# Optimization experiments

Hardware: AMD Instinct MI355X
Metric: run time of the kernel (lower is better)

Reference implementation:

```python
import jax, jax.numpy as jnp
import numpy as np

N = 100_000      # nodes
E = 1_600_000    # edges (avg degree 16)
IN_DIM = 128
HID = 512
NCLS = 64
BN_EPS = 1e-5


def setup_inputs() -> dict:
    key = jax.random.key(0)
    ks = jax.random.split(key, 16)

    def lin(k, fi, fo):
        kw, kb = jax.random.split(k)
        s = 1.0 / np.sqrt(fi)
        return (jax.random.uniform(kw, (fi, fo), jnp.float32, -s, s),
                jax.random.uniform(kb, (fo,), jnp.float32, -s, s))

    W1a, b1a = lin(ks[2], IN_DIM, HID)
    W1b, b1b = lin(ks[3], HID, HID)
    W2a, b2a = lin(ks[4], HID, HID)
    W2b, b2b = lin(ks[5], HID, NCLS)
    return {
        "x": jax.random.normal(ks[0], (N, IN_DIM), jnp.float32),
        "edge_index": jax.random.randint(ks[1], (2, E), 0, N, jnp.int32),
        "g": jnp.zeros((1,), jnp.int32),
        "A_k": jnp.zeros((1,), jnp.int32),
        "D": jnp.zeros((1,), jnp.int32),
        "Kindices": jnp.zeros((1,), jnp.int32),
        "de": jnp.zeros((1,), jnp.int32),
        "M": jnp.zeros((1,), jnp.int32),
        "I": jnp.zeros((1,), jnp.int32),
        "W1a": W1a, "b1a": b1a, "W1b": W1b, "b1b": b1b,
        "gamma1": jnp.ones((HID,), jnp.float32), "beta1": jnp.zeros((HID,), jnp.float32),
        "W2a": W2a, "b2a": b2a, "W2b": W2b, "b2b": b2b,
        "gamma2": jnp.ones((NCLS,), jnp.float32), "beta2": jnp.zeros((NCLS,), jnp.float32),
    }


def _gin_conv(x, src, dst, Wa, ba, Wb, bb):
    # PyG GINConv (eps=0): nn(x + sum_{j in N(i)} x_j); messages x[src] summed at dst
    agg = jax.ops.segment_sum(x[src], dst, num_segments=N)
    h = x + agg
    h = jax.nn.relu(h @ Wa + ba)
    return h @ Wb + bb


def _batchnorm(x, gamma, beta):
    # training-mode BatchNorm1d: batch stats over node dim, biased variance
    mu = jnp.mean(x, axis=0)
    var = jnp.mean(jnp.square(x - mu), axis=0)
    return gamma * (x - mu) * jax.lax.rsqrt(var + BN_EPS) + beta


def reference(x, edge_index, g, A_k, D, Kindices, de, M, I,
              W1a, b1a, W1b, b1b, gamma1, beta1,
              W2a, b2a, W2b, b2b, gamma2, beta2):
    src, dst = edge_index[0], edge_index[1]
    h = jax.nn.selu(_gin_conv(x, src, dst, W1a, b1a, W1b, b1b))
    h = _batchnorm(h, gamma1, beta1)
    # dropout(p=0.5) omitted (eval-mode / deterministic reference)
    h = jax.nn.selu(_gin_conv(h, src, dst, W2a, b2a, W2b, b2b))
    h = _batchnorm(h, gamma2, beta2)
    return jax.nn.softmax(h, axis=1)
```

## Files before the change

### kernel.cpp

```cpp
#include <hip/hip_runtime.h>
#include <hip/hip_bf16.h>

#define N_NODES 100000
#define N_EDGES 1600000
#define IN_DIM 128
#define HID 512
#define NCLS 64

typedef __attribute__((ext_vector_type(8))) short bf16x8;
typedef __attribute__((ext_vector_type(4))) float f32x4;

__device__ inline float bf2f(unsigned short b) {
    unsigned int u = ((unsigned int)b) << 16;
    return __builtin_bit_cast(float, u);
}
__device__ inline unsigned short f2bf(float f) {
    unsigned int u = __builtin_bit_cast(unsigned int, f);
    unsigned int lsb = (u >> 16) & 1u;
    u += 0x7fffu + lsb;
    return (unsigned short)(u >> 16);
}
__device__ inline float selu_f(float x) {
    const float scale = 1.0507009873554805f;
    const float alpha = 1.6732632423543772f;
    return x > 0.f ? scale * x : scale * alpha * (__expf(x) - 1.f);
}
__device__ inline void stb(float* p, float v) { *p = v; }
__device__ inline void stb(unsigned short* p, float v) { *p = f2bf(v); }

__device__ inline void gl_lds16(const void* g, void* l) {
    __builtin_amdgcn_global_load_lds((const __attribute__((address_space(1))) void*)g,
                                     (__attribute__((address_space(3))) void*)l, 16, 0, 0);
}

__global__ __launch_bounds__(256) void k_cast(const float* __restrict__ x,
                                              unsigned short* __restrict__ xb) {
    size_t g = (size_t)blockIdx.x * 256 + threadIdx.x;
    size_t total = (size_t)N_NODES * IN_DIM / 8;
    if (g >= total) return;
    const float4* p = (const float4*)(x + g * 8);
    float4 v0 = p[0], v1 = p[1];
    uint4 o;
    o.x = (unsigned)f2bf(v0.x) | ((unsigned)f2bf(v0.y) << 16);
    o.y = (unsigned)f2bf(v0.z) | ((unsigned)f2bf(v0.w) << 16);
    o.z = (unsigned)f2bf(v1.x) | ((unsigned)f2bf(v1.y) << 16);
    o.w = (unsigned)f2bf(v1.z) | ((unsigned)f2bf(v1.w) << 16);
    ((uint4*)xb)[g] = o;
}

__global__ __launch_bounds__(256) void k_deg(const int* __restrict__ dst, int* __restrict__ deg) {
    int e = blockIdx.x * 256 + threadIdx.x;
    if (e < N_EDGES) atomicAdd(&deg[dst[e]], 1);
}

#define SCAN_NB 98

__global__ __launch_bounds__(256) void k_scan_part(const int* __restrict__ deg, int* __restrict__ part) {
    __shared__ int sd[256];
    int b = blockIdx.x, t = threadIdx.x;
    int i0 = b * 1024 + t * 4;
    int s = 0;
#pragma unroll
    for (int k = 0; k < 4; ++k) if (i0 + k < N_NODES) s += deg[i0 + k];
    sd[t] = s;
    __syncthreads();
    for (int o = 128; o > 0; o >>= 1) {
        if (t < o) sd[t] += sd[t + o];
        __syncthreads();
    }
    if (t == 0) part[b] = sd[0];
}

__global__ __launch_bounds__(128) void k_scan_mid(const int* __restrict__ part, int* __restrict__ base,
                                                  int* __restrict__ off) {
    __shared__ int sp[128];
    int t = threadIdx.x;
    int v = (t < SCAN_NB) ? part[t] : 0;
    sp[t] = v;
    __syncthreads();
    for (int o = 1; o < 128; o <<= 1) {
        int tv = (t >= o) ? sp[t - o] : 0;
        __syncthreads();
        sp[t] += tv;
        __syncthreads();
    }
    if (t < SCAN_NB) base[t] = sp[t] - v;
    if (t == SCAN_NB - 1) off[N_NODES] = sp[t];
}

__global__ __launch_bounds__(256) void k_scan_fin(const int* __restrict__ deg, const int* __restrict__ base,
                                                  int* __restrict__ off, int* __restrict__ pos) {
    __shared__ int sd[256];
    int b = blockIdx.x, t = threadIdx.x;
    int i0 = b * 1024 + t * 4;
    int v[4]; int s = 0;
#pragma unroll
    for (int k = 0; k < 4; ++k) { v[k] = (i0 + k < N_NODES) ? deg[i0 + k] : 0; s += v[k]; }
    sd[t] = s;
    __syncthreads();
    for (int o = 1; o < 256; o <<= 1) {
        int tv = (t >= o) ? sd[t - o] : 0;
        __syncthreads();
        sd[t] += tv;
        __syncthreads();
    }
    int excl = base[b] + sd[t] - s;
#pragma unroll
    for (int k = 0; k < 4; ++k) {
        if (i0 + k < N_NODES) { off[i0 + k] = excl; pos[i0 + k] = excl; excl += v[k]; }
    }
}

__global__ __launch_bounds__(256) void k_fill(const int* __restrict__ src, const int* __restrict__ dst,
                                              int* __restrict__ pos, int* __restrict__ adj) {
    int e = blockIdx.x * 256 + threadIdx.x;
    if (e < N_EDGES) {
        int p = atomicAdd(&pos[dst[e]], 1);
        adj[p] = src[e];
    }
}

__global__ __launch_bounds__(256) void k_pack(const float* __restrict__ W,
                                              unsigned short* __restrict__ Wp, int K, int NC) {
    int idx = blockIdx.x * 256 + threadIdx.x;
    if (idx >= K * NC) return;
    int j = idx & 7;
    int l = (idx >> 3) & 63;
    int t = idx >> 9;
    int KT = K >> 5;
    int kt = t % KT;
    int nt = t / KT;
    int k = kt * 32 + (l >> 4) * 8 + j;
    int n = nt * 16 + (l & 15);
    Wp[idx] = f2bf(W[(size_t)k * NC + n]);
}

__global__ __launch_bounds__(256) void k_packT(const float* __restrict__ W,
                                               unsigned short* __restrict__ WT, int K, int NC) {
    int idx = blockIdx.x * 256 + threadIdx.x;
    if (idx >= K * NC) return;
    int k = idx & (K - 1);
    int n = idx / K;
    WT[idx] = f2bf(W[(size_t)k * NC + n]);
}

__global__ __launch_bounds__(256) void k_agg1(const unsigned short* __restrict__ xb,
                                              const int* __restrict__ off, const int* __restrict__ adj,
                                              unsigned short* __restrict__ A1) {
    int w = (blockIdx.x * 256 + threadIdx.x) >> 6;
    if (w >= N_NODES) return;
    int lane = threadIdx.x & 63;
    unsigned v = ((const unsigned*)(xb + (size_t)w * IN_DIM))[lane];
    float s0 = bf2f((unsigned short)(v & 0xffff));
    float s1 = bf2f((unsigned short)(v >> 16));
    int e0 = off[w], e1 = off[w + 1];
    int e = e0;
    for (; e + 4 <= e1; e += 4) {
        int j0 = adj[e], j1 = adj[e + 1], j2 = adj[e + 2], j3 = adj[e + 3];
        unsigned u0 = ((const unsigned*)(xb + (size_t)j0 * IN_DIM))[lane];
        unsigned u1 = ((const unsigned*)(xb + (size_t)j1 * IN_DIM))[lane];
        unsigned u2 = ((const unsigned*)(xb + (size_t)j2 * IN_DIM))[lane];
        unsigned u3 = ((const unsigned*)(xb + (size_t)j3 * IN_DIM))[lane];
        s0 += bf2f((unsigned short)(u0 & 0xffff)) + bf2f((unsigned short)(u1 & 0xffff)) +
              bf2f((unsigned short)(u2 & 0xffff)) + bf2f((unsigned short)(u3 & 0xffff));
        s1 += bf2f((unsigned short)(u0 >> 16)) + bf2f((unsigned short)(u1 >> 16)) +
              bf2f((unsigned short)(u2 >> 16)) + bf2f((unsigned short)(u3 >> 16));
    }
    for (; e < e1; ++e) {
        unsigned u = ((const unsigned*)(xb + (size_t)adj[e] * IN_DIM))[lane];
        s0 += bf2f((unsigned short)(u & 0xffff));
        s1 += bf2f((unsigned short)(u >> 16));
    }
    ((unsigned*)(A1 + (size_t)w * IN_DIM))[lane] = (unsigned)f2bf(s0) | ((unsigned)f2bf(s1) << 16);
}

__global__ __launch_bounds__(256) void k_aggbn2(const unsigned short* __restrict__ h,
                                                const int* __restrict__ off, const int* __restrict__ adj,
                                                const float* __restrict__ bn,
                                                unsigned short* __restrict__ outb) {
    int w = (blockIdx.x * 256 + threadIdx.x) >> 6;
    if (w >= N_NODES) return;
    int lane = threadIdx.x & 63;
    int fb = blockIdx.y * 256 + lane * 4;
    const unsigned short* hp = h + fb;
    float scl[4], shf[4];
#pragma unroll
    for (int k = 0; k < 4; ++k) {
        scl[k] = bn[2 * HID + fb + k];
        shf[k] = bn[3 * HID + fb + k];
    }
    uint2 v = *(const uint2*)(hp + (size_t)w * HID);
    float s0 = bf2f((unsigned short)(v.x & 0xffff));
    float s1 = bf2f((unsigned short)(v.x >> 16));
    float s2 = bf2f((unsigned short)(v.y & 0xffff));
    float s3 = bf2f((unsigned short)(v.y >> 16));
    int e0 = off[w], e1 = off[w + 1];
    int e = e0;
    for (; e + 4 <= e1; e += 4) {
        int j0 = adj[e], j1 = adj[e + 1], j2 = adj[e + 2], j3 = adj[e + 3];
        uint2 u0 = *(const uint2*)(hp + (size_t)j0 * HID);
        uint2 u1 = *(const uint2*)(hp + (size_t)j1 * HID);
        uint2 u2 = *(const uint2*)(hp + (size_t)j2 * HID);
        uint2 u3 = *(const uint2*)(hp + (size_t)j3 * HID);
        s0 += bf2f((unsigned short)(u0.x & 0xffff)) + bf2f((unsigned short)(u1.x & 0xffff)) +
              bf2f((unsigned short)(u2.x & 0xffff)) + bf2f((unsigned short)(u3.x & 0xffff));
        s1 += bf2f((unsigned short)(u0.x >> 16)) + bf2f((unsigned short)(u1.x >> 16)) +
              bf2f((unsigned short)(u2.x >> 16)) + bf2f((unsigned short)(u3.x >> 16));
        s2 += bf2f((unsigned short)(u0.y & 0xffff)) + bf2f((unsigned short)(u1.y & 0xffff)) +
              bf2f((unsigned short)(u2.y & 0xffff)) + bf2f((unsigned short)(u3.y & 0xffff));
        s3 += bf2f((unsigned short)(u0.y >> 16)) + bf2f((unsigned short)(u1.y >> 16)) +
              bf2f((unsigned short)(u2.y >> 16)) + bf2f((unsigned short)(u3.y >> 16));
    }
    for (; e < e1; ++e) {
        uint2 u = *(const uint2*)(hp + (size_t)adj[e] * HID);
        s0 += bf2f((unsigned short)(u.x & 0xffff));
        s1 += bf2f((unsigned short)(u.x >> 16));
        s2 += bf2f((unsigned short)(u.y & 0xffff));
        s3 += bf2f((unsigned short)(u.y >> 16));
    }
    float dp1 = (float)(e1 - e0 + 1);
    float r0 = s0 * scl[0] + dp1 * shf[0];
    float r1 = s1 * scl[1] + dp1 * shf[1];
    float r2 = s2 * scl[2] + dp1 * shf[2];
    float r3 = s3 * scl[3] + dp1 * shf[3];
    unsigned long long o =
        (unsigned long long)((unsigned)f2bf(r0) | ((unsigned)f2bf(r1) << 16)) |
        ((unsigned long long)((unsigned)f2bf(r2) | ((unsigned)f2bf(r3) << 16)) << 32);
    __builtin_nontemporal_store(o, (unsigned long long*)(outb + (size_t)w * HID + fb));
}

template <int K, int ACT>
__global__ __launch_bounds__(256) void k_tgemm(const unsigned short* __restrict__ A,
                                               const unsigned short* __restrict__ WT,
                                               const float* __restrict__ bias,
                                               unsigned short* __restrict__ Out, int M) {
    constexpr int NC = 512;
    __shared__ __align__(16) char smem[32768];
    const int tid = threadIdx.x;
    const int lane = tid & 63;
    const int w = tid >> 6;
    const int wm = w >> 1, wn = w & 1;
    const int l15 = lane & 15, lg = lane >> 4;
    const int rowbase = blockIdx.y * 128;
    const int colbase = blockIdx.x * 128;

    f32x4 acc[4][4];
#pragma unroll
    for (int i = 0; i < 4; ++i)
#pragma unroll
        for (int j = 0; j < 4; ++j) acc[i][j] = (f32x4)0.f;

    for (int k0 = 0; k0 < K; k0 += 64) {
#pragma unroll
        for (int i = 0; i < 4; ++i) {
            int slot = i * 256 + tid;
            int r = slot >> 3;
            int u = (slot & 7) ^ (r & 7);
            int gr = rowbase + r; if (gr >= M) gr = M - 1;
            gl_lds16(A + (size_t)gr * K + k0 + u * 8, smem + (i * 256 + w * 64) * 16);
        }
#pragma unroll
        for (int i = 0; i < 4; ++i) {
            int slot = i * 256 + tid;
            int c = slot >> 3;
            int u = (slot & 7) ^ (c & 7);
            gl_lds16(WT + (size_t)(colbase + c) * K + k0 + u * 8,
                     smem + 16384 + (i * 256 + w * 64) * 16);
        }
        __syncthreads();
#pragma unroll
        for (int kin = 0; kin < 2; ++kin) {
            bf16x8 af[4], bfr[4];
#pragma unroll
            for (int mi = 0; mi < 4; ++mi) {
                int r = wm * 64 + mi * 16 + l15;
                int u = (kin * 4 + lg) ^ (r & 7);
                af[mi] = *(const bf16x8*)(smem + r * 128 + u * 16);
            }
#pragma unroll
            for (int ni = 0; ni < 4; ++ni) {
                int c = wn * 64 + ni * 16 + l15;
                int u = (kin * 4 + lg) ^ (c & 7);
                bfr[ni] = *(const bf16x8*)(smem + 16384 + c * 128 + u * 16);
            }
#pragma unroll
            for (int mi = 0; mi < 4; ++mi)
#pragma unroll
                for (int ni = 0; ni < 4; ++ni)
                    acc[mi][ni] = __builtin_amdgcn_mfma_f32_16x16x32_bf16(af[mi], bfr[ni], acc[mi][ni], 0, 0, 0);
        }
        __syncthreads();
    }

#pragma unroll
    for (int ni = 0; ni < 4; ++ni) {
        int c = wn * 64 + ni * 16 + l15;
        float bv = bias[colbase + c];
#pragma unroll
        for (int mi = 0; mi < 4; ++mi) {
#pragma unroll
            for (int r = 0; r < 4; ++r) {
                int row = wm * 64 + mi * 16 + lg * 4 + r;
                float t = acc[mi][ni][r] + bv;
                t = (ACT == 0) ? fmaxf(t, 0.f) : selu_f(t);
                int byte = (row * 256 + c * 2) ^ ((row & 7) << 4);
                *(unsigned short*)(smem + byte) = f2bf(t);
            }
        }
    }
    __syncthreads();
#pragma unroll
    for (int it = 0; it < 8; ++it) {
        int idx = it * 256 + tid;
        int row = idx >> 4;
        int ch = idx & 15;
        int gr = rowbase + row;
        if (gr < M) {
            uint4 v = *(const uint4*)(smem + row * 256 + ((ch ^ (row & 7)) << 4));
            *(uint4*)(Out + (size_t)gr * NC + colbase + ch * 8) = v;
        }
    }
}

template <int K, int NC, int ACT, int WAVES_M, int WAVES_N, int NFRAG, typename TOUT>
__global__ __launch_bounds__(WAVES_M * WAVES_N * 64) void k_mgemm(
    const unsigned short* __restrict__ A, const unsigned short* __restrict__ Wp,
    const float* __restrict__ bias, TOUT* __restrict__ Out, int M) {
    const int tid = threadIdx.x;
    const int lane = tid & 63;
    const int w = tid >> 6;
    const int wm = w / WAVES_N;
    const int wn = w % WAVES_N;
    const int l15 = lane & 15;
    const int lg = lane >> 4;
    const int rowbase = blockIdx.x * (32 * WAVES_M) + wm * 32;
    const int colbase = blockIdx.y * (WAVES_N * 16 * NFRAG) + wn * 16 * NFRAG;
    int r0 = rowbase + l15; if (r0 > M - 1) r0 = M - 1;
    int r1 = rowbase + 16 + l15; if (r1 > M - 1) r1 = M - 1;
    const unsigned short* pa0 = A + (size_t)r0 * K + lg * 8;
    const unsigned short* pa1 = A + (size_t)r1 * K + lg * 8;
    const unsigned short* pw = Wp + (size_t)(colbase >> 4) * (K / 32) * 512 + lane * 8;

    f32x4 acc[2][NFRAG];
#pragma unroll
    for (int i = 0; i < 2; ++i)
#pragma unroll
        for (int j = 0; j < NFRAG; ++j) acc[i][j] = (f32x4)0.f;

#pragma unroll 2
    for (int kt = 0; kt < K / 32; ++kt) {
        bf16x8 a0 = *(const bf16x8*)(pa0 + kt * 32);
        bf16x8 a1 = *(const bf16x8*)(pa1 + kt * 32);
#pragma unroll
        for (int ni = 0; ni < NFRAG; ++ni) {
            bf16x8 bv = *(const bf16x8*)(pw + (ni * (K / 32) + kt) * 512);
            acc[0][ni] = __builtin_amdgcn_mfma_f32_16x16x32_bf16(a0, bv, acc[0][ni], 0, 0, 0);
            acc[1][ni] = __builtin_amdgcn_mfma_f32_16x16x32_bf16(a1, bv, acc[1][ni], 0, 0, 0);
        }
    }

#pragma unroll
    for (int ni = 0; ni < NFRAG; ++ni) {
        int c = colbase + ni * 16 + l15;
        float bv = bias[c];
#pragma unroll
        for (int mi = 0; mi < 2; ++mi) {
#pragma unroll
            for (int r = 0; r < 4; ++r) {
                int row = rowbase + mi * 16 + lg * 4 + r;
                if (row < M) {
                    float t = acc[mi][ni][r] + bv;
                    t = (ACT == 0) ? fmaxf(t, 0.f) : selu_f(t);
                    stb(&Out[(size_t)row * NC + c], t);
                }
            }
        }
    }
}

__global__ __launch_bounds__(256) void k_bnstats_h(const unsigned short* __restrict__ C,
                                                   float* __restrict__ sums) {
    int t = threadIdx.x;
    float s0 = 0, q0 = 0, s1 = 0, q1 = 0;
    for (int r = blockIdx.x; r < N_NODES; r += gridDim.x) {
        unsigned v = ((const unsigned*)(C + (size_t)r * HID))[t];
        float a = bf2f((unsigned short)(v & 0xffff));
        float b = bf2f((unsigned short)(v >> 16));
        s0 += a; q0 += a * a;
        s1 += b; q1 += b * b;
    }
    atomicAdd(&sums[2 * t], s0);
    atomicAdd(&sums[2 * t + 1], s1);
    atomicAdd(&sums[HID + 2 * t], q0);
    atomicAdd(&sums[HID + 2 * t + 1], q1);
}

__global__ void k_bnprep(float* __restrict__ bn, const float* __restrict__ gamma,
                         const float* __restrict__ beta, int C, float invn) {
    int c = threadIdx.x + blockIdx.x * blockDim.x;
    if (c >= C) return;
    float mu = bn[c] * invn;
    float var = bn[C + c] * invn - mu * mu;
    float sc = gamma[c] * rsqrtf(var + 1e-5f);
    bn[2 * C + c] = sc;
    bn[3 * C + c] = beta[c] - mu * sc;
}

__global__ __launch_bounds__(256) void k_bnstats_o(const float* __restrict__ O,
                                                   float* __restrict__ bn2) {
    int t = threadIdx.x;
    int c = t & 63;
    int rr = t >> 6;
    float s = 0, q = 0;
    for (int r = blockIdx.x * 4 + rr; r < N_NODES; r += gridDim.x * 4) {
        float a = O[(size_t)r * NCLS + c];
        s += a; q += a * a;
    }
    atomicAdd(&bn2[c], s);
    atomicAdd(&bn2[NCLS + c], q);
}

__global__ __launch_bounds__(256) void k_softmax(float* __restrict__ O, const float* __restrict__ bn2) {
    int w = (blockIdx.x * 256 + threadIdx.x) >> 6;
    if (w >= N_NODES) return;
    int lane = threadIdx.x & 63;
    float z = O[(size_t)w * NCLS + lane] * bn2[2 * NCLS + lane] + bn2[3 * NCLS + lane];
    float m = z;
#pragma unroll
    for (int o = 32; o > 0; o >>= 1) m = fmaxf(m, __shfl_xor(m, o));
    float e = __expf(z - m);
    float s = e;
#pragma unroll
    for (int o = 32; o > 0; o >>= 1) s += __shfl_xor(s, o);
    O[(size_t)w * NCLS + lane] = e / s;
}

extern "C" void kernel_launch(void* const* d_in, const int* in_sizes, int n_in,
                              void* d_out, int out_size, void* d_ws, size_t ws_size,
                              hipStream_t stream) {
    const float* x = (const float*)d_in[0];
    const int* edge = (const int*)d_in[1];
    const int* srcp = edge;
    const int* dstp = edge + N_EDGES;
    const float* W1a = (const float*)d_in[9];
    const float* b1a = (const float*)d_in[10];
    const float* W1b = (const float*)d_in[11];
    const float* b1b = (const float*)d_in[12];
    const float* gamma1 = (const float*)d_in[13];
    const float* beta1 = (const float*)d_in[14];
    const float* W2a = (const float*)d_in[15];
    const float* b2a = (const float*)d_in[16];
    const float* W2b = (const float*)d_in[17];
    const float* b2b = (const float*)d_in[18];
    const float* gamma2 = (const float*)d_in[19];
    const float* beta2 = (const float*)d_in[20];
    float* out = (float*)d_out;

    char* ws = (char*)d_ws;
    size_t o = 0;
    auto alloc = [&](size_t bytes) -> char* {
        char* p = ws + o;
        o = (o + bytes + 255) & ~(size_t)255;
        return p;
    };
    int* off = (int*)alloc((N_NODES + 1) * sizeof(int));
    int* deg = (int*)alloc(N_NODES * sizeof(int));
    int* pos = (int*)alloc(N_NODES * sizeof(int));
    int* adj = (int*)alloc(N_EDGES * sizeof(int));
    int* part = (int*)alloc(SCAN_NB * sizeof(int));
    int* base = (int*)alloc(SCAN_NB * sizeof(int));
    float* bn1 = (float*)alloc(4 * HID * sizeof(float));
    float* bn2 = (float*)alloc(4 * NCLS * sizeof(float));
    unsigned short* WT1 = (unsigned short*)alloc((size_t)IN_DIM * HID * sizeof(unsigned short));
    unsigned short* WT2 = (unsigned short*)alloc((size_t)HID * HID * sizeof(unsigned short));
    unsigned short* WT3 = (unsigned short*)alloc((size_t)HID * HID * sizeof(unsigned short));
    unsigned short* Wp4 = (unsigned short*)alloc((size_t)HID * NCLS * sizeof(unsigned short));
    unsigned short* xb = (unsigned short*)alloc((size_t)N_NODES * IN_DIM * sizeof(unsigned short));
    unsigned short* A1 = (unsigned short*)alloc((size_t)N_NODES * IN_DIM * sizeof(unsigned short));
    unsigned short* B = (unsigned short*)alloc((size_t)N_NODES * HID * sizeof(unsigned short));
    unsigned short* C = (unsigned short*)alloc((size_t)N_NODES * HID * sizeof(unsigned short));

    hipMemsetAsync(deg, 0, N_NODES * sizeof(int), stream);
    hipMemsetAsync(bn1, 0, 2 * HID * sizeof(float), stream);
    hipMemsetAsync(bn2, 0, 2 * NCLS * sizeof(float), stream);

    int eb = (N_EDGES + 255) / 256;
    k_cast<<<(N_NODES * IN_DIM / 8 + 255) / 256, 256, 0, stream>>>(x, xb);
    k_deg<<<eb, 256, 0, stream>>>(dstp, deg);
    k_scan_part<<<SCAN_NB, 256, 0, stream>>>(deg, part);
    k_scan_mid<<<1, 128, 0, stream>>>(part, base, off);
    k_scan_fin<<<SCAN_NB, 256, 0, stream>>>(deg, base, off, pos);
    k_fill<<<eb, 256, 0, stream>>>(srcp, dstp, pos, adj);

    k_packT<<<(IN_DIM * HID) / 256, 256, 0, stream>>>(W1a, WT1, IN_DIM, HID);
    k_packT<<<(HID * HID) / 256, 256, 0, stream>>>(W1b, WT2, HID, HID);
    k_packT<<<(HID * HID) / 256, 256, 0, stream>>>(W2a, WT3, HID, HID);
    k_pack<<<(HID * NCLS) / 256, 256, 0, stream>>>(W2b, Wp4, HID, NCLS);

    int nwb = (N_NODES * 64 + 255) / 256;
    int mb128 = (N_NODES + 127) / 128;

    k_agg1<<<nwb, 256, 0, stream>>>(xb, off, adj, A1);
    k_tgemm<IN_DIM, 0><<<dim3(4, mb128), 256, 0, stream>>>(A1, WT1, b1a, B, N_NODES);
    k_tgemm<HID, 1><<<dim3(4, mb128), 256, 0, stream>>>(B, WT2, b1b, C, N_NODES);

    k_bnstats_h<<<1024, 256, 0, stream>>>(C, bn1);
    k_bnprep<<<2, 256, 0, stream>>>(bn1, gamma1, beta1, HID, 1.0f / N_NODES);

    k_aggbn2<<<dim3(nwb, 2), 256, 0, stream>>>(C, off, adj, bn1, B);

    k_tgemm<HID, 0><<<dim3(4, mb128), 256, 0, stream>>>(B, WT3, b2a, C, N_NODES);
    k_mgemm<HID, NCLS, 1, 8, 1, 4, float><<<dim3((N_NODES + 255) / 256, 1), 512, 0, stream>>>(C, Wp4, b2b, out, N_NODES);

    k_bnstats_o<<<1024, 256, 0, stream>>>(out, bn2);
    k_bnprep<<<1, 64, 0, stream>>>(bn2, gamma2, beta2, NCLS, 1.0f / N_NODES);
    k_softmax<<<nwb, 256, 0, stream>>>(out, bn2);
}
```

Measured before the change: 1.018 ms.

## Fuse BatchNorm statistics into GEMM epilogues, sort adjacency, remap GEMM grid

Batch-norm sum and sum-of-squares are now accumulated in the epilogues of the hidden GEMM and the output GEMM. This removes the two standalone stats passes that re-read C and the output, and adds a small reduction kernel for the hidden-layer partials. The adjacency lists of each node are sorted by source index with a per-thread insertion sort, so gathers hit memory in a more local order. The tiled GEMM uses a 1D grid with an 8-row-block swizzle so neighbouring blocks share A tiles in L2. Costs are an extra sort kernel, a scratch buffer for the partials, and stats computed from fp32 values before bf16 rounding.

New measurement: 881.5 us. 1.15x faster.

```diff
diff --git a/kernel.cpp b/kernel.cpp
--- a/kernel.cpp
+++ b/kernel.cpp
@@ -9,6 +9,10 @@
 
 typedef __attribute__((ext_vector_type(8))) short bf16x8;
 typedef __attribute__((ext_vector_type(4))) float f32x4;
+
+#define RB_COUNT 782
+#define RB_PAD 784
+#define TG_GRID (RB_PAD * 4)
 
 __device__ inline float bf2f(unsigned short b) {
     unsigned int u = ((unsigned int)b) << 16;
@@ -118,6 +122,27 @@
         int p = atomicAdd(&pos[dst[e]], 1);
         adj[p] = src[e];
     }
+}
+
+__global__ __launch_bounds__(256) void k_sortadj(const int* __restrict__ off, int* __restrict__ adj) {
+    __shared__ int sb[64 * 256];
+    int n = blockIdx.x * 256 + threadIdx.x;
+    if (n >= N_NODES) return;
+    int t = threadIdx.x;
+    int e0 = off[n], e1 = off[n + 1];
+    int d = e1 - e0;
+    if (d <= 1 || d > 64) return;
+    for (int i = 0; i < d; ++i) sb[i * 256 + t] = adj[e0 + i];
+    for (int i = 1; i < d; ++i) {
+        int key = sb[i * 256 + t];
+        int j = i - 1;
+        while (j >= 0 && sb[j * 256 + t] > key) {
+            sb[(j + 1) * 256 + t] = sb[j * 256 + t];
+            --j;
+        }
+        sb[(j + 1) * 256 + t] = key;
+    }
+    for (int i = 0; i < d; ++i) adj[e0 + i] = sb[i * 256 + t];
 }
 
 __global__ __launch_bounds__(256) void k_pack(const float* __restrict__ W,
@@ -229,20 +254,28 @@
     __builtin_nontemporal_store(o, (unsigned long long*)(outb + (size_t)w * HID + fb));
 }
 
-template <int K, int ACT>
+template <int K, int ACT, int STATS>
 __global__ __launch_bounds__(256) void k_tgemm(const unsigned short* __restrict__ A,
                                                const unsigned short* __restrict__ WT,
                                                const float* __restrict__ bias,
-                                               unsigned short* __restrict__ Out, int M) {
+                                               unsigned short* __restrict__ Out,
+                                               float* __restrict__ scratch, int M) {
     constexpr int NC = 512;
-    __shared__ __align__(16) char smem[32768];
+    __shared__ __align__(16) char smem[32768 + 2048];
+    const int bid = blockIdx.x;
+    const int r8 = bid & 7;
+    const int q = bid >> 3;
+    const int cb = q & 3;
+    const int rb = (q >> 2) * 8 + r8;
+    const int rowbase = rb * 128;
+    const int colbase = cb * 128;
+    if (rowbase >= M) return;
+
     const int tid = threadIdx.x;
     const int lane = tid & 63;
     const int w = tid >> 6;
     const int wm = w >> 1, wn = w & 1;
     const int l15 = lane & 15, lg = lane >> 4;
-    const int rowbase = blockIdx.y * 128;
-    const int colbase = blockIdx.x * 128;
 
     f32x4 acc[4][4];
 #pragma unroll
@@ -292,6 +325,11 @@
         __syncthreads();
     }
 
+    float cs[4], cq[4];
+    if (STATS) {
+#pragma unroll
+        for (int ni = 0; ni < 4; ++ni) { cs[ni] = 0.f; cq[ni] = 0.f; }
+    }
 #pragma unroll
     for (int ni = 0; ni < 4; ++ni) {
         int c = wn * 64 + ni * 16 + l15;
@@ -303,8 +341,23 @@
                 int row = wm * 64 + mi * 16 + lg * 4 + r;
                 float t = acc[mi][ni][r] + bv;
                 t = (ACT == 0) ? fmaxf(t, 0.f) : selu_f(t);
+                if (STATS && (rowbase + row < M)) { cs[ni] += t; cq[ni] += t * t; }
                 int byte = (row * 256 + c * 2) ^ ((row & 7) << 4);
                 *(unsigned short*)(smem + byte) = f2bf(t);
+            }
+        }
+    }
+    if (STATS) {
+        float* sS = (float*)(smem + 32768);
+#pragma unroll
+        for (int ni = 0; ni < 4; ++ni) {
+            float a = cs[ni];
+            a += __shfl_xor(a, 16); a += __shfl_xor(a, 32);
+            float b = cq[ni];
+            b += __shfl_xor(b, 16); b += __shfl_xor(b, 32);
+            if (lg == 0) {
+                sS[wm * 256 + (wn * 64 + ni * 16 + l15)] = a;
+                sS[wm * 256 + 128 + (wn * 64 + ni * 16 + l15)] = b;
             }
         }
     }
@@ -320,12 +373,34 @@
             *(uint4*)(Out + (size_t)gr * NC + colbase + ch * 8) = v;
         }
     }
-}
-
-template <int K, int NC, int ACT, int WAVES_M, int WAVES_N, int NFRAG, typename TOUT>
+    if (STATS) {
+        const float* sS = (const float*)(smem + 32768);
+        int c = tid & 127, kind = tid >> 7;
+        float v = sS[kind * 128 + c] + sS[256 + kind * 128 + c];
+        scratch[(size_t)(rb * 4 + cb) * 256 + kind * 128 + c] = v;
+    }
+}
+
+__global__ __launch_bounds__(256) void k_bnred(const float* __restrict__ scratch,
+                                               float* __restrict__ bn) {
+    int t = threadIdx.x;
+    float loc[4] = {0.f, 0.f, 0.f, 0.f};
+    for (int rb = blockIdx.x; rb < RB_COUNT; rb += gridDim.x) {
+#pragma unroll
+        for (int cbk = 0; cbk < 4; ++cbk)
+            loc[cbk] += scratch[(size_t)(rb * 4 + cbk) * 256 + t];
+    }
+    int kind = t >> 7, cl = t & 127;
+#pragma unroll
+    for (int cbk = 0; cbk < 4; ++cbk)
+        atomicAdd(&bn[kind * HID + cbk * 128 + cl], loc[cbk]);
+}
+
+template <int K, int NC, int ACT, int WAVES_M, int WAVES_N, int NFRAG, int STATS, typename TOUT>
 __global__ __launch_bounds__(WAVES_M * WAVES_N * 64) void k_mgemm(
     const unsigned short* __restrict__ A, const unsigned short* __restrict__ Wp,
-    const float* __restrict__ bias, TOUT* __restrict__ Out, int M) {
+    const float* __restrict__ bias, TOUT* __restrict__ Out, float* __restrict__ bnacc, int M) {
+    __shared__ float sS[WAVES_M * WAVES_N * 128];
     const int tid = threadIdx.x;
     const int lane = tid & 63;
     const int w = tid >> 6;
@@ -359,6 +434,11 @@
         }
     }
 
+    float cs[NFRAG], cq[NFRAG];
+    if (STATS) {
+#pragma unroll
+        for (int ni = 0; ni < NFRAG; ++ni) { cs[ni] = 0.f; cq[ni] = 0.f; }
+    }
 #pragma unroll
     for (int ni = 0; ni < NFRAG; ++ni) {
         int c = colbase + ni * 16 + l15;
@@ -371,28 +451,32 @@
                 if (row < M) {
                     float t = acc[mi][ni][r] + bv;
                     t = (ACT == 0) ? fmaxf(t, 0.f) : selu_f(t);
+                    if (STATS) { cs[ni] += t; cq[ni] += t * t; }
                     stb(&Out[(size_t)row * NC + c], t);
                 }
             }
         }
     }
-}
-
-__global__ __launch_bounds__(256) void k_bnstats_h(const unsigned short* __restrict__ C,
-                                                   float* __restrict__ sums) {
-    int t = threadIdx.x;
-    float s0 = 0, q0 = 0, s1 = 0, q1 = 0;
-    for (int r = blockIdx.x; r < N_NODES; r += gridDim.x) {
-        unsigned v = ((const unsigned*)(C + (size_t)r * HID))[t];
-        float a = bf2f((unsigned short)(v & 0xffff));
-        float b = bf2f((unsigned short)(v >> 16));
-        s0 += a; q0 += a * a;
-        s1 += b; q1 += b * b;
-    }
-    atomicAdd(&sums[2 * t], s0);
-    atomicAdd(&sums[2 * t + 1], s1);
-    atomicAdd(&sums[HID + 2 * t], q0);
-    atomicAdd(&sums[HID + 2 * t + 1], q1);
+    if (STATS) {
+#pragma unroll
+        for (int ni = 0; ni < NFRAG; ++ni) {
+            float a = cs[ni];
+            a += __shfl_xor(a, 16); a += __shfl_xor(a, 32);
+            float b = cq[ni];
+            b += __shfl_xor(b, 16); b += __shfl_xor(b, 32);
+            if (lg == 0) {
+                sS[w * 128 + (ni * 16 + l15)] = a;
+                sS[w * 128 + 64 + (ni * 16 + l15)] = b;
+            }
+        }
+        __syncthreads();
+        if (tid < 128) {
+            float v = 0.f;
+#pragma unroll
+            for (int ww = 0; ww < WAVES_M * WAVES_N; ++ww) v += sS[ww * 128 + tid];
+            atomicAdd(&bnacc[tid], v);
+        }
+    }
 }
 
 __global__ void k_bnprep(float* __restrict__ bn, const float* __restrict__ gamma,
@@ -404,20 +488,6 @@
     float sc = gamma[c] * rsqrtf(var + 1e-5f);
     bn[2 * C + c] = sc;
     bn[3 * C + c] = beta[c] - mu * sc;
-}
-
-__global__ __launch_bounds__(256) void k_bnstats_o(const float* __restrict__ O,
-                                                   float* __restrict__ bn2) {
-    int t = threadIdx.x;
-    int c = t & 63;
-    int rr = t >> 6;
-    float s = 0, q = 0;
-    for (int r = blockIdx.x * 4 + rr; r < N_NODES; r += gridDim.x * 4) {
-        float a = O[(size_t)r * NCLS + c];
-        s += a; q += a * a;
-    }
-    atomicAdd(&bn2[c], s);
-    atomicAdd(&bn2[NCLS + c], q);
 }
 
 __global__ __launch_bounds__(256) void k_softmax(float* __restrict__ O, const float* __restrict__ bn2) {
@@ -471,6 +541,7 @@
     int* base = (int*)alloc(SCAN_NB * sizeof(int));
     float* bn1 = (float*)alloc(4 * HID * sizeof(float));
     float* bn2 = (float*)alloc(4 * NCLS * sizeof(float));
+    float* stat = (float*)alloc((size_t)RB_COUNT * 4 * 256 * sizeof(float));
     unsigned short* WT1 = (unsigned short*)alloc((size_t)IN_DIM * HID * sizeof(unsigned short));
     unsigned short* WT2 = (unsigned short*)alloc((size_t)HID * HID * sizeof(unsigned short));
     unsigned short* WT3 = (unsigned short*)alloc((size_t)HID * HID * sizeof(unsigned short));
@@ -491,6 +562,7 @@
     k_scan_mid<<<1, 128, 0, stream>>>(part, base, off);
     k_scan_fin<<<SCAN_NB, 256, 0, stream>>>(deg, base, off, pos);
     k_fill<<<eb, 256, 0, stream>>>(srcp, dstp, pos, adj);
+    k_sortadj<<<(N_NODES + 255) / 256, 256, 0, stream>>>(off, adj);
 
     k_packT<<<(IN_DIM * HID) / 256, 256, 0, stream>>>(W1a, WT1, IN_DIM, HID);
     k_packT<<<(HID * HID) / 256, 256, 0, stream>>>(W1b, WT2, HID, HID);
@@ -498,21 +570,17 @@
     k_pack<<<(HID * NCLS) / 256, 256, 0, stream>>>(W2b, Wp4, HID, NCLS);
 
     int nwb = (N_NODES * 64 + 255) / 256;
-    int mb128 = (N_NODES + 127) / 128;
 
     k_agg1<<<nwb, 256, 0, stream>>>(xb, off, adj, A1);
-    k_tgemm<IN_DIM, 0><<<dim3(4, mb128), 256, 0, stream>>>(A1, WT1, b1a, B, N_NODES);
-    k_tgemm<HID, 1><<<dim3(4, mb128), 256, 0, stream>>>(B, WT2, b1b, C, N_NODES);
-
-    k_bnstats_h<<<1024, 256, 0, stream>>>(C, bn1);
+    k_tgemm<IN_DIM, 0, 0><<<TG_GRID, 256, 0, stream>>>(A1, WT1, b1a, B, nullptr, N_NODES);
+    k_tgemm<HID, 1, 1><<<TG_GRID, 256, 0, stream>>>(B, WT2, b1b, C, stat, N_NODES);
+    k_bnred<<<32, 256, 0, stream>>>(stat, bn1);
     k_bnprep<<<2, 256, 0, stream>>>(bn1, gamma1, beta1, HID, 1.0f / N_NODES);
 
     k_aggbn2<<<dim3(nwb, 2), 256, 0, stream>>>(C, off, adj, bn1, B);
-
-    k_tgemm<HID, 0><<<dim3(4, mb128), 256, 0, stream>>>(B, WT3, b2a, C, N_NODES);
-    k_mgemm<HID, NCLS, 1, 8, 1, 4, float><<<dim3((N_NODES + 255) / 256, 1), 512, 0, stream>>>(C, Wp4, b2b, out, N_NODES);
-
-    k_bnstats_o<<<1024, 256, 0, stream>>>(out, bn2);
+    k_tgemm<HID, 0, 0><<<TG_GRID, 256, 0, stream>>>(B, WT3, b2a, C, nullptr, N_NODES);
+    k_mgemm<HID, NCLS, 1, 8, 1, 4, 1, float><<<dim3((N_NODES + 255) / 256, 1), 512, 0, stream>>>(C, Wp4, b2b, out, bn2, N_NODES);
+
     k_bnprep<<<1, 64, 0, stream>>>(bn2, gamma2, beta2, NCLS, 1.0f / N_NODES);
     k_softmax<<<nwb, 256, 0, stream>>>(out, bn2);
 }
```
